# Optimization experiments

Hardware: AMD Instinct MI355X
Metric: run time of the kernel (lower is better)

Reference implementation:

```python
import jax, jax.numpy as jnp
import numpy as np
from jax import lax

# Model hyperparameters (match init_kwargs + Mamba2 defaults: ngroups=1, d_conv=4)
B_, IN_DIM, L_ = 4, 128, 2048
D_MODEL, OUT_DIM, D_STATE, K_SAME = 256, 128, 16, 4
EXPAND, HEADDIM, D_CONV = 3, 3, 4
D_INNER = EXPAND * D_MODEL            # 768
NHEADS = D_INNER // HEADDIM           # 256
CONV_DIM = D_INNER + 2 * D_STATE      # 800 (x, B, C go through depthwise conv)
D_IN_PROJ = 2 * D_INNER + 2 * D_STATE + NHEADS  # 1824 (z, xBC, dt)
EPS = 1e-5
DN = ('NCH', 'OIH', 'NCH')


def setup_inputs() -> dict:
    key = jax.random.key(0)
    ks = jax.random.split(key, 12)
    s = lambda f: 1.0 / np.sqrt(f)
    x = jax.random.normal(ks[0], (B_, IN_DIM, L_), jnp.float32)
    conv_w = jax.random.normal(ks[1], (D_MODEL, IN_DIM, K_SAME), jnp.float32) * s(IN_DIM * K_SAME)
    conv_b = jax.random.normal(ks[2], (D_MODEL,), jnp.float32) * 0.02
    in_proj_w = jax.random.normal(ks[3], (D_MODEL, D_IN_PROJ), jnp.float32) * s(D_MODEL)
    dw_conv_w = jax.random.normal(ks[4], (CONV_DIM, D_CONV), jnp.float32) * s(D_CONV)
    dw_conv_b = jax.random.normal(ks[5], (CONV_DIM,), jnp.float32) * 0.02
    dt_bias = jax.random.normal(ks[6], (NHEADS,), jnp.float32) * 0.5
    A_log = jnp.log(jax.random.uniform(ks[7], (NHEADS,), jnp.float32, 1.0, 16.0))
    D = 1.0 + jax.random.normal(ks[8], (NHEADS,), jnp.float32) * 0.1
    norm_w = jnp.ones((D_INNER,), jnp.float32)
    mamba_out_w = jax.random.normal(ks[9], (D_INNER, D_MODEL), jnp.float32) * s(D_INNER)
    out_conv_w = jax.random.normal(ks[10], (OUT_DIM, D_MODEL, K_SAME), jnp.float32) * s(D_MODEL * K_SAME)
    return dict(x=x, conv_w=conv_w, conv_b=conv_b, in_proj_w=in_proj_w,
                dw_conv_w=dw_conv_w, dw_conv_b=dw_conv_b, dt_bias=dt_bias,
                A_log=A_log, D=D, norm_w=norm_w, mamba_out_w=mamba_out_w,
                out_conv_w=out_conv_w)


def _ssd_scan(dt, A, Bm, Cm, xs):
    """Selective state-space recurrence.
    dt: [B,L,H]  A: [H]  Bm,Cm: [B,L,N]  xs: [B,L,H,P]  ->  y: [B,L,H,P]"""
    dA = jnp.exp(dt * A)  # [B,L,H]

    def step(h, inp):  # h: [B,H,P,N]
        dA_t, dt_t, B_t, C_t, x_t = inp
        dBx = (dt_t[:, :, None] * x_t)[..., None] * B_t[:, None, None, :]  # [B,H,P,N]
        h = h * dA_t[:, :, None, None] + dBx
        y = jnp.einsum('bhpn,bn->bhp', h, C_t)
        return h, y

    inputs = (dA.transpose(1, 0, 2), dt.transpose(1, 0, 2),
              Bm.transpose(1, 0, 2), Cm.transpose(1, 0, 2), xs.transpose(1, 0, 2, 3))
    h0 = jnp.zeros((dt.shape[0], NHEADS, HEADDIM, D_STATE), dt.dtype)
    _, ys = lax.scan(step, h0, inputs)
    return ys.transpose(1, 0, 2, 3)


def reference(x, conv_w, conv_b, in_proj_w, dw_conv_w, dw_conv_b, dt_bias,
              A_log, D, norm_w, mamba_out_w, out_conv_w):
    B, _, L = x.shape
    # Conv1d padding='same' with even kernel k=4: torch pads (left=1, right=2)
    h = lax.conv_general_dilated(x, conv_w, (1,), [(1, 2)], dimension_numbers=DN)
    h = h + conv_b[None, :, None]
    u = h.transpose(0, 2, 1)  # [B,L,d_model]

    zxbcdt = u @ in_proj_w  # [B,L,1824]
    z = zxbcdt[..., :D_INNER]
    xBC = zxbcdt[..., D_INNER:D_INNER + CONV_DIM]
    dt = zxbcdt[..., D_INNER + CONV_DIM:]  # [B,L,H]
    dt = jax.nn.softplus(dt + dt_bias)

    # causal depthwise conv over xBC, then silu
    xBC_c = lax.conv_general_dilated(xBC.transpose(0, 2, 1), dw_conv_w[:, None, :], (1,),
                                     [(D_CONV - 1, 0)], feature_group_count=CONV_DIM,
                                     dimension_numbers=DN)
    xBC = jax.nn.silu((xBC_c + dw_conv_b[None, :, None]).transpose(0, 2, 1))
    xs = xBC[..., :D_INNER].reshape(B, L, NHEADS, HEADDIM)
    Bm = xBC[..., D_INNER:D_INNER + D_STATE]
    Cm = xBC[..., D_INNER + D_STATE:]

    A = -jnp.exp(A_log)
    y = _ssd_scan(dt, A, Bm, Cm, xs) + D[None, None, :, None] * xs  # [B,L,H,P]
    y = y.reshape(B, L, D_INNER)

    # gated RMSNorm (norm_before_gate=False): gate first, then normalize
    y = y * jax.nn.silu(z)
    y = y * lax.rsqrt(jnp.mean(y * y, axis=-1, keepdims=True) + EPS) * norm_w

    out = (y @ mamba_out_w).transpose(0, 2, 1)  # [B,d_model,L]
    out = lax.conv_general_dilated(out, out_conv_w, (1,), [(1, 2)], dimension_numbers=DN)
    return out
```

## Files before the change

### kernel.cpp

```cpp
#include <hip/hip_runtime.h>
#include <math.h>

#define B_      4
#define L_      2048
#define IN_DIM  128
#define D_MODEL 256
#define OUT_DIM 128
#define D_STATE 16
#define D_INNER 768
#define NHEADS  256
#define HEADDIM 3
#define CONV_DIM 800
#define D_IN_PROJ 1824
#define DT_START (D_INNER + CONV_DIM)

#define SCAN_NC 32
#define SCAN_CL 64
#define LPAD    2051

typedef short  short8 __attribute__((ext_vector_type(8)));
typedef float  f32x4  __attribute__((ext_vector_type(4)));

__device__ __forceinline__ unsigned short f2bf(float f) {
    unsigned int u = __float_as_uint(f);
    u = (u + 0x7fffu + ((u >> 16) & 1u)) >> 16;
    return (unsigned short)u;
}
__device__ __forceinline__ float bf2f(unsigned short h) {
    return __uint_as_float(((unsigned int)h) << 16);
}

__global__ __launch_bounds__(256) void prep_all_kernel(
    unsigned short* __restrict__ xh, unsigned short* __restrict__ xl,
    const float* __restrict__ cw, unsigned short* __restrict__ cwh,
    unsigned short* __restrict__ cwl,
    const float* __restrict__ x,
    const float* __restrict__ ipsrc, unsigned short* __restrict__ ipwh,
    unsigned short* __restrict__ ipwl,
    const float* __restrict__ cow, unsigned short* __restrict__ cowh,
    unsigned short* __restrict__ th,
    const float* __restrict__ mosrc, unsigned short* __restrict__ mowh,
    unsigned short* __restrict__ mowl)
{
    __shared__ float tile[32][33];
    int bid = blockIdx.x;
    if (bid < 6) {
        int t = bid * 256 + threadIdx.x;
        int n = B_ * 3 * IN_DIM;
        if (t < n) {
            int ch = t % IN_DIM, rb = t / IN_DIM;
            int b = rb / 3, ri = rb % 3;
            int row = (ri == 0) ? 0 : (ri == 1) ? (L_ + 1) : (L_ + 2);
            size_t off = ((size_t)b * LPAD + row) * IN_DIM + ch;
            xh[off] = 0; xl[off] = 0;
        }
    } else if (bid < 518) {
        int t = (bid - 6) * 256 + threadIdx.x;
        if (t < D_MODEL * 512) {
            int o = t >> 9, kk = t & 511;
            int k = kk >> 7, i = kk & 127;
            float v = cw[((size_t)o * IN_DIM + i) * 4 + k];
            unsigned short h = f2bf(v);
            cwh[t] = h; cwl[t] = f2bf(v - bf2f(h));
        }
    } else if (bid < 1542) {
        int tid = bid - 518;
        int b = tid >> 8;
        int l0 = (tid & 63) * 32, i0 = ((tid >> 6) & 3) * 32;
        int tx = threadIdx.x & 31, ty = threadIdx.x >> 5;
        const float* xb = x + (size_t)b * IN_DIM * L_;
        #pragma unroll
        for (int r = 0; r < 4; ++r)
            tile[ty + r * 8][tx] = xb[(size_t)(i0 + ty + r * 8) * L_ + l0 + tx];
        __syncthreads();
        #pragma unroll
        for (int r = 0; r < 4; ++r) {
            int l = l0 + ty + r * 8;
            float v = tile[tx][ty + r * 8];
            size_t off = ((size_t)b * LPAD + l + 1) * IN_DIM + i0 + tx;
            unsigned short h = f2bf(v);
            xh[off] = h;
            xl[off] = f2bf(v - bf2f(h));
        }
    } else if (bid < 1998) {
        int tid = bid - 1542;
        int n0 = (tid % 57) * 32, k0 = (tid / 57) * 32;
        const int K = D_MODEL, N = D_IN_PROJ;
        int tx = threadIdx.x & 31, ty = threadIdx.x >> 5;
        #pragma unroll
        for (int r = 0; r < 4; ++r)
            tile[ty + r * 8][tx] = ipsrc[(size_t)(k0 + ty + r * 8) * N + n0 + tx];
        __syncthreads();
        #pragma unroll
        for (int r = 0; r < 4; ++r) {
            int n = n0 + ty + r * 8;
            float v = tile[tx][ty + r * 8];
            unsigned short h = f2bf(v);
            ipwh[(size_t)n * K + k0 + tx] = h;
            ipwl[(size_t)n * K + k0 + tx] = f2bf(v - bf2f(h));
        }
    } else if (bid < 2510) {
        int t = (bid - 1998) * 256 + threadIdx.x;
        if (t < OUT_DIM * 1024) {
            int o = t >> 10, kk = t & 1023;
            int k = kk >> 8, c = kk & 255;
            cowh[t] = f2bf(cow[((size_t)o * D_MODEL + c) * 4 + k]);
        }
    } else if (bid < 2522) {
        int t = (bid - 2510) * 256 + threadIdx.x;
        int n = B_ * 3 * D_MODEL;
        if (t < n) {
            int ch = t % D_MODEL, rb = t / D_MODEL;
            int b = rb / 3, ri = rb % 3;
            int row = (ri == 0) ? 0 : (ri == 1) ? (L_ + 1) : (L_ + 2);
            size_t off = ((size_t)b * LPAD + row) * D_MODEL + ch;
            th[off] = 0;
        }
    } else {
        int tid = bid - 2522;
        int n0 = (tid & 7) * 32, k0 = (tid >> 3) * 32;
        const int K = D_INNER, N = D_MODEL;
        int tx = threadIdx.x & 31, ty = threadIdx.x >> 5;
        #pragma unroll
        for (int r = 0; r < 4; ++r)
            tile[ty + r * 8][tx] = mosrc[(size_t)(k0 + ty + r * 8) * N + n0 + tx];
        __syncthreads();
        #pragma unroll
        for (int r = 0; r < 4; ++r) {
            int n = n0 + ty + r * 8;
            float v = tile[tx][ty + r * 8];
            unsigned short h = f2bf(v);
            mowh[(size_t)n * K + k0 + tx] = h;
            mowl[(size_t)n * K + k0 + tx] = f2bf(v - bf2f(h));
        }
    }
}

__global__ __launch_bounds__(256) void gemm_ip2_kernel(
    const unsigned short* __restrict__ Ah, const unsigned short* __restrict__ Al,
    const unsigned short* __restrict__ Bh, const unsigned short* __restrict__ Bl,
    float* __restrict__ C, int M, int N, int K)
{
    __shared__ __align__(16) unsigned short AsH[128][40];
    __shared__ __align__(16) unsigned short AsL[128][40];
    __shared__ __align__(16) unsigned short BsH[128][40];
    __shared__ __align__(16) unsigned short BsL[128][40];

    int m0 = blockIdx.y * 128, n0 = blockIdx.x * 128;
    int t = threadIdx.x;
    int wid = t >> 6, lane = t & 63;
    int wm = (wid >> 1) * 64, wn = (wid & 1) * 64;
    int fr = lane & 15, fq = lane >> 4;
    bool full = (n0 + 127 >= DT_START);

    f32x4 z4 = {0.f, 0.f, 0.f, 0.f};
    f32x4 acc[4][4];
    #pragma unroll
    for (int i = 0; i < 4; ++i)
        #pragma unroll
        for (int j = 0; j < 4; ++j) acc[i][j] = z4;

    if (!full) {
        for (int k0 = 0; k0 < K; k0 += 32) {
            __syncthreads();
            #pragma unroll
            for (int p = 0; p < 2; ++p) {
                int idx = p * 256 + t;
                int row = idx >> 2, q = idx & 3;
                int koff = k0 + q * 8;
                *(float4*)&AsH[row][q * 8] =
                    *(const float4*)(Ah + (size_t)(m0 + row) * K + koff);
                int n = n0 + row;
                *(float4*)&BsH[row][q * 8] =
                    *(const float4*)(Bh + (size_t)n * K + koff);
            }
            __syncthreads();

            short8 ah[4], bh[4];
            #pragma unroll
            for (int i = 0; i < 4; ++i) {
                ah[i] = *(const short8*)&AsH[wm + i * 16 + fr][fq * 8];
                bh[i] = *(const short8*)&BsH[wn + i * 16 + fr][fq * 8];
            }
            #pragma unroll
            for (int i = 0; i < 4; ++i)
                #pragma unroll
                for (int j = 0; j < 4; ++j)
                    acc[i][j] = __builtin_amdgcn_mfma_f32_16x16x32_bf16(
                        ah[i], bh[j], acc[i][j], 0, 0, 0);
        }
    } else {
        for (int k0 = 0; k0 < K; k0 += 32) {
            __syncthreads();
            #pragma unroll
            for (int p = 0; p < 2; ++p) {
                int idx = p * 256 + t;
                int row = idx >> 2, q = idx & 3;
                int koff = k0 + q * 8;
                *(float4*)&AsH[row][q * 8] =
                    *(const float4*)(Ah + (size_t)(m0 + row) * K + koff);
                *(float4*)&AsL[row][q * 8] =
                    *(const float4*)(Al + (size_t)(m0 + row) * K + koff);
                int n = n0 + row;
                float4 vbh = make_float4(0.f, 0.f, 0.f, 0.f), vbl = vbh;
                if (n < N) {
                    vbh = *(const float4*)(Bh + (size_t)n * K + koff);
                    vbl = *(const float4*)(Bl + (size_t)n * K + koff);
                }
                *(float4*)&BsH[row][q * 8] = vbh;
                *(float4*)&BsL[row][q * 8] = vbl;
            }
            __syncthreads();

            short8 ah[4], al[4], bh[4], bl[4];
            #pragma unroll
            for (int i = 0; i < 4; ++i) {
                ah[i] = *(const short8*)&AsH[wm + i * 16 + fr][fq * 8];
                al[i] = *(const short8*)&AsL[wm + i * 16 + fr][fq * 8];
                bh[i] = *(const short8*)&BsH[wn + i * 16 + fr][fq * 8];
                bl[i] = *(const short8*)&BsL[wn + i * 16 + fr][fq * 8];
            }
            #pragma unroll
            for (int i = 0; i < 4; ++i)
                #pragma unroll
                for (int j = 0; j < 4; ++j) {
                    acc[i][j] = __builtin_amdgcn_mfma_f32_16x16x32_bf16(
                        ah[i], bh[j], acc[i][j], 0, 0, 0);
                    acc[i][j] = __builtin_amdgcn_mfma_f32_16x16x32_bf16(
                        ah[i], bl[j], acc[i][j], 0, 0, 0);
                    acc[i][j] = __builtin_amdgcn_mfma_f32_16x16x32_bf16(
                        al[i], bh[j], acc[i][j], 0, 0, 0);
                }
        }
    }

    #pragma unroll
    for (int i = 0; i < 4; ++i) {
        int r0 = m0 + wm + i * 16 + fq * 4;
        #pragma unroll
        for (int j = 0; j < 4; ++j) {
            int cc = n0 + wn + j * 16 + fr;
            if (cc < N) {
                #pragma unroll
                for (int r = 0; r < 4; ++r)
                    C[(size_t)(r0 + r) * N + cc] = acc[i][j][r];
            }
        }
    }
}

__global__ __launch_bounds__(256) void gemm_ci_kernel(
    const unsigned short* __restrict__ Ah, const unsigned short* __restrict__ Al,
    const unsigned short* __restrict__ Bh, const unsigned short* __restrict__ Bl,
    const float* __restrict__ bias,
    unsigned short* __restrict__ Ch, unsigned short* __restrict__ Cl)
{
    const int K = 512;
    __shared__ __align__(16) unsigned short AsH[64][40];
    __shared__ __align__(16) unsigned short AsL[64][40];
    __shared__ __align__(16) unsigned short BsH[128][40];
    __shared__ __align__(16) unsigned short BsL[128][40];

    int m0 = blockIdx.y * 64, n0 = blockIdx.x * 128;
    int b = m0 >> 11;
    size_t abase = ((size_t)b * LPAD + (m0 & 2047)) * IN_DIM;
    int t = threadIdx.x;
    int wid = t >> 6, lane = t & 63;
    int wm = (wid >> 1) * 32, wn = (wid & 1) * 64;
    int fr = lane & 15, fq = lane >> 4;
    int rr = t >> 2, q = t & 3;

    f32x4 z4 = {0.f, 0.f, 0.f, 0.f};
    f32x4 acc[2][4];
    #pragma unroll
    for (int i = 0; i < 2; ++i)
        #pragma unroll
        for (int j = 0; j < 4; ++j) acc[i][j] = z4;

    float4 rAh, rAl, rBh0, rBh1, rBl0, rBl1;
    auto ld = [&](int k0) {
        int koff = k0 + q * 8;
        rAh = *(const float4*)(Ah + abase + (size_t)rr * IN_DIM + koff);
        rAl = *(const float4*)(Al + abase + (size_t)rr * IN_DIM + koff);
        rBh0 = *(const float4*)(Bh + (size_t)(n0 + rr) * K + koff);
        rBh1 = *(const float4*)(Bh + (size_t)(n0 + rr + 64) * K + koff);
        rBl0 = *(const float4*)(Bl + (size_t)(n0 + rr) * K + koff);
        rBl1 = *(const float4*)(Bl + (size_t)(n0 + rr + 64) * K + koff);
    };
    ld(0);

    for (int k0 = 0; k0 < K; k0 += 32) {
        __syncthreads();
        *(float4*)&AsH[rr][q * 8] = rAh;
        *(float4*)&AsL[rr][q * 8] = rAl;
        *(float4*)&BsH[rr][q * 8] = rBh0;
        *(float4*)&BsH[rr + 64][q * 8] = rBh1;
        *(float4*)&BsL[rr][q * 8] = rBl0;
        *(float4*)&BsL[rr + 64][q * 8] = rBl1;
        __syncthreads();
        if (k0 + 32 < K) ld(k0 + 32);

        short8 ah[2], al[2], bh[4], bl[4];
        #pragma unroll
        for (int i = 0; i < 2; ++i) {
            ah[i] = *(const short8*)&AsH[wm + i * 16 + fr][fq * 8];
            al[i] = *(const short8*)&AsL[wm + i * 16 + fr][fq * 8];
        }
        #pragma unroll
        for (int j = 0; j < 4; ++j) {
            bh[j] = *(const short8*)&BsH[wn + j * 16 + fr][fq * 8];
            bl[j] = *(const short8*)&BsL[wn + j * 16 + fr][fq * 8];
        }
        #pragma unroll
        for (int i = 0; i < 2; ++i)
            #pragma unroll
            for (int j = 0; j < 4; ++j) {
                acc[i][j] = __builtin_amdgcn_mfma_f32_16x16x32_bf16(
                    ah[i], bh[j], acc[i][j], 0, 0, 0);
                acc[i][j] = __builtin_amdgcn_mfma_f32_16x16x32_bf16(
                    ah[i], bl[j], acc[i][j], 0, 0, 0);
                acc[i][j] = __builtin_amdgcn_mfma_f32_16x16x32_bf16(
                    al[i], bh[j], acc[i][j], 0, 0, 0);
            }
    }

    #pragma unroll
    for (int i = 0; i < 2; ++i) {
        int r0 = m0 + wm + i * 16 + fq * 4;
        #pragma unroll
        for (int j = 0; j < 4; ++j) {
            int cc = n0 + wn + j * 16 + fr;
            float bc = bias[cc];
            #pragma unroll
            for (int r = 0; r < 4; ++r) {
                float v = acc[i][j][r] + bc;
                unsigned short h = f2bf(v);
                size_t off = (size_t)(r0 + r) * D_MODEL + cc;
                Ch[off] = h;
                Cl[off] = f2bf(v - bf2f(h));
            }
        }
    }
}

__global__ __launch_bounds__(256) void gemm_mo_kernel(
    const unsigned short* __restrict__ Ah, const unsigned short* __restrict__ Bh,
    unsigned short* __restrict__ Ch)
{
    const int K = D_INNER;
    __shared__ __align__(16) unsigned short AsH[64][40];
    __shared__ __align__(16) unsigned short BsH[128][40];

    int m0 = blockIdx.y * 64, n0 = blockIdx.x * 128;
    int t = threadIdx.x;
    int wid = t >> 6, lane = t & 63;
    int wm = (wid >> 1) * 32, wn = (wid & 1) * 64;
    int fr = lane & 15, fq = lane >> 4;
    int rr = t >> 2, q = t & 3;

    f32x4 z4 = {0.f, 0.f, 0.f, 0.f};
    f32x4 acc[2][4];
    #pragma unroll
    for (int i = 0; i < 2; ++i)
        #pragma unroll
        for (int j = 0; j < 4; ++j) acc[i][j] = z4;

    float4 rA, rB0, rB1;
    auto ld = [&](int k0) {
        int koff = k0 + q * 8;
        rA  = *(const float4*)(Ah + (size_t)(m0 + rr) * K + koff);
        rB0 = *(const float4*)(Bh + (size_t)(n0 + rr) * K + koff);
        rB1 = *(const float4*)(Bh + (size_t)(n0 + rr + 64) * K + koff);
    };
    ld(0);

    for (int k0 = 0; k0 < K; k0 += 32) {
        __syncthreads();
        *(float4*)&AsH[rr][q * 8] = rA;
        *(float4*)&BsH[rr][q * 8] = rB0;
        *(float4*)&BsH[rr + 64][q * 8] = rB1;
        __syncthreads();
        if (k0 + 32 < K) ld(k0 + 32);

        short8 ah[2], bh[4];
        #pragma unroll
        for (int i = 0; i < 2; ++i)
            ah[i] = *(const short8*)&AsH[wm + i * 16 + fr][fq * 8];
        #pragma unroll
        for (int j = 0; j < 4; ++j)
            bh[j] = *(const short8*)&BsH[wn + j * 16 + fr][fq * 8];
        #pragma unroll
        for (int i = 0; i < 2; ++i)
            #pragma unroll
            for (int j = 0; j < 4; ++j)
                acc[i][j] = __builtin_amdgcn_mfma_f32_16x16x32_bf16(
                    ah[i], bh[j], acc[i][j], 0, 0, 0);
    }

    int b = m0 >> 11;
    #pragma unroll
    for (int i = 0; i < 2; ++i) {
        int r0 = m0 + wm + i * 16 + fq * 4;
        #pragma unroll
        for (int j = 0; j < 4; ++j) {
            int cc = n0 + wn + j * 16 + fr;
            #pragma unroll
            for (int r = 0; r < 4; ++r) {
                int l = (r0 + r) & 2047;
                size_t off = ((size_t)b * LPAD + l + 1) * D_MODEL + cc;
                Ch[off] = f2bf(acc[i][j][r]);
            }
        }
    }
}

__global__ __launch_bounds__(256) void gemm_co_kernel(
    const unsigned short* __restrict__ Ah, const unsigned short* __restrict__ Bh,
    float* __restrict__ out)
{
    const int K = 1024;
    __shared__ __align__(16) unsigned short AsH[64][40];
    __shared__ __align__(16) unsigned short BsH[64][40];
    __shared__ __align__(16) float outT[64][68];

    int m0 = blockIdx.y * 64, n0 = blockIdx.x * 64;
    int b = m0 >> 11, l0t = m0 & 2047;
    size_t abase = ((size_t)b * LPAD + l0t) * D_MODEL;
    int t = threadIdx.x;
    int wid = t >> 6, lane = t & 63;
    int wm = (wid >> 1) * 32, wn = (wid & 1) * 32;
    int fr = lane & 15, fq = lane >> 4;
    int rr = t >> 2, q = t & 3;

    f32x4 z4 = {0.f, 0.f, 0.f, 0.f};
    f32x4 acc[2][2];
    #pragma unroll
    for (int i = 0; i < 2; ++i)
        #pragma unroll
        for (int j = 0; j < 2; ++j) acc[i][j] = z4;

    float4 rA, rB;
    auto ld = [&](int k0) {
        int koff = k0 + q * 8;
        rA = *(const float4*)(Ah + abase + (size_t)rr * D_MODEL + koff);
        rB = *(const float4*)(Bh + (size_t)(n0 + rr) * K + koff);
    };
    ld(0);

    for (int k0 = 0; k0 < K; k0 += 32) {
        __syncthreads();
        *(float4*)&AsH[rr][q * 8] = rA;
        *(float4*)&BsH[rr][q * 8] = rB;
        __syncthreads();
        if (k0 + 32 < K) ld(k0 + 32);

        short8 ah[2], bh[2];
        #pragma unroll
        for (int i = 0; i < 2; ++i)
            ah[i] = *(const short8*)&AsH[wm + i * 16 + fr][fq * 8];
        #pragma unroll
        for (int j = 0; j < 2; ++j)
            bh[j] = *(const short8*)&BsH[wn + j * 16 + fr][fq * 8];
        #pragma unroll
        for (int i = 0; i < 2; ++i)
            #pragma unroll
            for (int j = 0; j < 2; ++j)
                acc[i][j] = __builtin_amdgcn_mfma_f32_16x16x32_bf16(
                    ah[i], bh[j], acc[i][j], 0, 0, 0);
    }

    #pragma unroll
    for (int i = 0; i < 2; ++i)
        #pragma unroll
        for (int j = 0; j < 2; ++j)
            *(float4*)&outT[wn + j * 16 + fr][wm + i * 16 + fq * 4] =
                make_float4(acc[i][j][0], acc[i][j][1],
                            acc[i][j][2], acc[i][j][3]);
    __syncthreads();
    #pragma unroll
    for (int e = 0; e < 4; ++e) {
        int idx = e * 256 + t;
        int rowl = idx >> 4, colp = (idx & 15) * 4;
        float* dst = out + ((size_t)(b * OUT_DIM + n0 + rowl)) * L_ + l0t + colp;
        *(float4*)dst = *(const float4*)&outT[rowl][colp];
    }
}

__global__ __launch_bounds__(256) void dwconv_kernel(
    const float* __restrict__ zx, const float* __restrict__ w,
    const float* __restrict__ bias, float* __restrict__ xBCs)
{
    int idx = blockIdx.x * 256 + threadIdx.x;
    int c   = idx % CONV_DIM;
    int bl8 = idx / CONV_DIM;
    int b  = bl8 >> 8;
    int l0 = (bl8 & 255) * 8;
    float4 wv = *(const float4*)&w[c * 4];
    float bi = bias[c];
    const float* base = zx + ((size_t)(b * L_ + l0)) * D_IN_PROJ + D_INNER + c;
    float r[11];
    #pragma unroll
    for (int k = 0; k < 11; ++k) {
        int l = l0 - 3 + k;
        r[k] = (l >= 0) ? base[(ptrdiff_t)(k - 3) * D_IN_PROJ] : 0.f;
    }
    #pragma unroll
    for (int i = 0; i < 8; ++i) {
        float acc = bi;
        acc = fmaf(r[i + 0], wv.x, acc);
        acc = fmaf(r[i + 1], wv.y, acc);
        acc = fmaf(r[i + 2], wv.z, acc);
        acc = fmaf(r[i + 3], wv.w, acc);
        float s = acc / (1.f + expf(-acc));
        xBCs[((size_t)(b * L_ + l0 + i)) * CONV_DIM + c] = s;
    }
}

__device__ __forceinline__ void scan_decode(int bid, int& b, int& c, int& hg)
{
    int bcl = bid & 7;
    hg = (bid >> 3) & 31;
    int bc = ((bid >> 8) << 3) | bcl;
    c = bc & 31;
    b = bc >> 5;
}

__global__ __launch_bounds__(512) void scan_local2g(
    const float* __restrict__ xBCs, const float* __restrict__ zx,
    const float* __restrict__ dt_bias, const float* __restrict__ A_log,
    float* __restrict__ Sloc, float* __restrict__ prodA,
    float* __restrict__ dtb, float* __restrict__ G)
{
    int bid = blockIdx.x;
    int t = threadIdx.x;
    if (bid < 128) {
        __shared__ float Bs[64][16];
        __shared__ float Csg[64][16];
        int c = bid & 31, b = bid >> 5;
        int row0 = b * L_ + c * SCAN_CL;
        if (t < 256) {
            int j = t >> 2, q = t & 3;
            const float* r = xBCs + (size_t)(row0 + j) * CONV_DIM + D_INNER;
            *(float4*)&Bs[j][q * 4] = *(const float4*)(r + q * 4);
            *(float4*)&Csg[j][q * 4] = *(const float4*)(r + D_STATE + q * 4);
        }
        __syncthreads();
        if (t < 256) {
            int i = t >> 2, jq = t & 3;
            float4 c0 = *(const float4*)&Csg[i][0];
            float4 c1 = *(const float4*)&Csg[i][4];
            float4 c2 = *(const float4*)&Csg[i][8];
            float4 c3 = *(const float4*)&Csg[i][12];
            float dot[16];
            #pragma unroll
            for (int jj = 0; jj < 16; ++jj) {
                int j = jq * 16 + jj;
                float4 b0 = *(const float4*)&Bs[j][0];
                float4 b1 = *(const float4*)&Bs[j][4];
                float4 b2 = *(const float4*)&Bs[j][8];
                float4 b3 = *(const float4*)&Bs[j][12];
                float d = c0.x * b0.x + c0.y * b0.y + c0.z * b0.z + c0.w * b0.w;
                d = fmaf(c1.x, b1.x, d); d = fmaf(c1.y, b1.y, d);
                d = fmaf(c1.z, b1.z, d); d = fmaf(c1.w, b1.w, d);
                d = fmaf(c2.x, b2.x, d); d = fmaf(c2.y, b2.y, d);
                d = fmaf(c2.z, b2.z, d); d = fmaf(c2.w, b2.w, d);
                d = fmaf(c3.x, b3.x, d); d = fmaf(c3.y, b3.y, d);
                d = fmaf(c3.z, b3.z, d); d = fmaf(c3.w, b3.w, d);
                dot[jj] = d;
            }
            float* gout = G + ((size_t)bid * 64 + i) * 64 + jq * 16;
            #pragma unroll
            for (int q = 0; q < 4; ++q)
                *(float4*)(gout + q * 4) =
                    make_float4(dot[q*4], dot[q*4+1], dot[q*4+2], dot[q*4+3]);
        }
        return;
    }

    __shared__ float  BsT[16][68];
    __shared__ __align__(16) float4 PkC4L[8][66];
    __shared__ float  UT[8][3][64];
    int b, c, hg;
    scan_decode(bid - 128, b, c, hg);
    int h0 = hg * 8;
    int row0 = b * L_ + c * SCAN_CL;

    if (t < 256) {
        int j = t >> 2, q = t & 3;
        const float* r = xBCs + (size_t)(row0 + j) * CONV_DIM;
        float4 bv = *(const float4*)(r + D_INNER + q * 4);
        BsT[q*4+0][j] = bv.x; BsT[q*4+1][j] = bv.y;
        BsT[q*4+2][j] = bv.z; BsT[q*4+3][j] = bv.w;
    }
    {
        int hh = t & 7, j = t >> 3;
        float v = zx[(size_t)(row0 + j) * D_IN_PROJ + DT_START + h0 + hh]
                  + dt_bias[h0 + hh];
        float dtv = (v > 20.f) ? v : log1pf(expf(v));
        dtb[(size_t)(row0 + j) * NHEADS + h0 + hh] = dtv;
        const float* xr = xBCs + (size_t)(row0 + j) * CONV_DIM + (h0 + hh) * 3;
        PkC4L[hh][j] = make_float4(dtv * xr[0], dtv * xr[1], dtv * xr[2], dtv);
    }
    __syncthreads();

    int wv = t >> 6, lane = t & 63;
    int hh = wv;
    int hhu = __builtin_amdgcn_readfirstlane(wv);
    int p = lane >> 4, n = lane & 15;
    int pc = (p < 3) ? p : 2;

    float4 own = PkC4L[hh][lane];
    float pkx = own.x, pky = own.y, pkz = own.z, pkw = own.w;
    float A = -__expf(A_log[h0 + hhu]);
    float cum = pkw * A;
    #pragma unroll
    for (int off = 1; off < 64; off <<= 1) {
        float sv = __shfl_up(cum, off);
        if (lane >= off) cum += sv;
    }
    float cum63 = __shfl(cum, 63);
    float wf = __expf(cum63 - cum);
    UT[hh][0][lane] = wf * pkx;
    UT[hh][1][lane] = wf * pky;
    UT[hh][2][lane] = wf * pkz;
    float state = 0.f;
    #pragma unroll
    for (int q = 0; q < 16; ++q) {
        float4 Bv = *(const float4*)&BsT[n][q * 4];
        float4 Uv = *(const float4*)&UT[hh][pc][q * 4];
        state = fmaf(Uv.x, Bv.x, state);
        state = fmaf(Uv.y, Bv.y, state);
        state = fmaf(Uv.z, Bv.z, state);
        state = fmaf(Uv.w, Bv.w, state);
    }
    size_t bh = (size_t)(b * NHEADS + h0 + hh);
    if (p < 3) Sloc[(bh * SCAN_NC + c) * 48 + p * 16 + n] = state;
    if (lane == 0) prodA[bh * SCAN_NC + c] = __expf(cum63);
}

__global__ __launch_bounds__(256) void scan_prefix_kernel(
    float* __restrict__ Sloc, const float* __restrict__ prodA)
{
    int wv   = blockIdx.x * 4 + (threadIdx.x >> 6);
    int lane = threadIdx.x & 63;
    int p = lane >> 4, n = lane & 15;
    bool act = (p < 3);
    int l48 = ((p < 3) ? p : 2) * 16 + n;
    size_t base = (size_t)wv * SCAN_NC;

    float cur = 0.f;
    for (int c = 0; c < SCAN_NC; ++c) {
        float s  = Sloc[(base + c) * 48 + l48];
        float pa = prodA[base + c];
        if (act) Sloc[(base + c) * 48 + l48] = cur;
        cur = fmaf(pa, cur, s);
    }
}

__global__ __launch_bounds__(512) void scan_final2(
    const float* __restrict__ xBCs, const float* __restrict__ dtb,
    const float* __restrict__ A_log, const float* __restrict__ Dp,
    const float* __restrict__ Sinit, const float* __restrict__ G,
    float* __restrict__ y)
{
    __shared__ __align__(16) float4 PkC4[8][67];
    __shared__ float XWx[8][64];
    __shared__ float XWy[8][64];
    __shared__ float XWz[8][64];
    __shared__ __align__(16) float Cs[64][36];
    union GsYsr {
        float gs[64][64];
        float ysr[64][25];
    };
    __shared__ __align__(16) GsYsr Us;
    int b, c, hg;
    scan_decode(blockIdx.x, b, c, hg);
    int h0 = hg * 8;
    int t = threadIdx.x;
    int row0 = b * L_ + c * SCAN_CL;

    {
        int hh = t & 7, j = t >> 3;
        float dtv = dtb[(size_t)(row0 + j) * NHEADS + h0 + hh];
        const float* xr = xBCs + (size_t)(row0 + j) * CONV_DIM + (h0 + hh) * 3;
        PkC4[hh][j + (j >> 4)] =
            make_float4(dtv * xr[0], dtv * xr[1], dtv * xr[2], dtv);
    }
    if (t < 256) {
        int j = t >> 2, q = t & 3;
        const float* r = xBCs + (size_t)(row0 + j) * CONV_DIM + D_INNER + D_STATE;
        *(float4*)&Cs[j][q * 4] = *(const float4*)(r + q * 4);
    }
    {
        const float* Gsrc = G + (size_t)(b * SCAN_NC + c) * 4096;
        #pragma unroll
        for (int e = 0; e < 2; ++e) {
            int idx = e * 512 + t;
            int row = idx >> 4, cq = (idx & 15) * 4;
            *(float4*)&Us.gs[row][cq ^ ((row & 7) << 2)] =
                *(const float4*)(Gsrc + (size_t)idx * 4);
        }
    }
    __syncthreads();

    int wv = t >> 6, lane = t & 63;
    int hh = wv;
    int hhu = __builtin_amdgcn_readfirstlane(wv);
    int I = lane >> 4;
    int sw = (lane & 7) << 2;

    float4 own = PkC4[hh][lane + (lane >> 4)];
    float pkx = own.x, pky = own.y, pkz = own.z, pkw = own.w;

    const float* sinp = Sinit +
        ((size_t)(b * NHEADS + h0 + hhu) * SCAN_NC + c) * 48;
    float A = -__expf(A_log[h0 + hhu]);
    float Dh = Dp[h0 + hhu];

    float cum = pkw * A;
    #pragma unroll
    for (int off = 1; off < 64; off <<= 1) {
        float sv = __shfl_up(cum, off);
        if (lane >= off) cum += sv;
    }
    float e0 = __shfl(cum, 15);
    float e1 = __shfl(cum, 31);
    float e2 = __shfl(cum, 47);
    float e3 = __shfl(cum, 63);
    int ia = (I << 4) - 1;
    float AIr = __shfl(cum, ia < 0 ? 0 : ia);
    float AI = (I == 0) ? 0.f : AIr;
    float ri = __expf(cum - AI);
    float Eo = (I == 0) ? e0 : (I == 1) ? e1 : (I == 2) ? e2 : e3;
    float wj = __expf(Eo - cum);
    XWx[hh][lane] = wj * pkx;
    XWy[hh][lane] = wj * pky;
    XWz[hh][lane] = wj * pkz;
    PkC4[hh][lane + (lane >> 4)].w = cum;
    float S0 = (I > 0) ? __expf(AI - e0) : 0.f;
    float S1 = (I > 1) ? __expf(AI - e1) : 0.f;
    float S2 = (I > 2) ? __expf(AI - e2) : 0.f;
    float ecum = __expf(cum);

    float4 c0 = *(const float4*)&Cs[lane][0];
    float4 c1 = *(const float4*)&Cs[lane][4];
    float4 c2 = *(const float4*)&Cs[lane][8];
    float4 c3 = *(const float4*)&Cs[lane][12];

    float s0, s1, s2;
    {
        s0 = c0.x*sinp[0];  s0 = fmaf(c0.y,sinp[1],s0);  s0 = fmaf(c0.z,sinp[2],s0);  s0 = fmaf(c0.w,sinp[3],s0);
        s0 = fmaf(c1.x,sinp[4],s0);  s0 = fmaf(c1.y,sinp[5],s0);  s0 = fmaf(c1.z,sinp[6],s0);  s0 = fmaf(c1.w,sinp[7],s0);
        s0 = fmaf(c2.x,sinp[8],s0);  s0 = fmaf(c2.y,sinp[9],s0);  s0 = fmaf(c2.z,sinp[10],s0); s0 = fmaf(c2.w,sinp[11],s0);
        s0 = fmaf(c3.x,sinp[12],s0); s0 = fmaf(c3.y,sinp[13],s0); s0 = fmaf(c3.z,sinp[14],s0); s0 = fmaf(c3.w,sinp[15],s0);
        s1 = c0.x*sinp[16]; s1 = fmaf(c0.y,sinp[17],s1); s1 = fmaf(c0.z,sinp[18],s1); s1 = fmaf(c0.w,sinp[19],s1);
        s1 = fmaf(c1.x,sinp[20],s1); s1 = fmaf(c1.y,sinp[21],s1); s1 = fmaf(c1.z,sinp[22],s1); s1 = fmaf(c1.w,sinp[23],s1);
        s1 = fmaf(c2.x,sinp[24],s1); s1 = fmaf(c2.y,sinp[25],s1); s1 = fmaf(c2.z,sinp[26],s1); s1 = fmaf(c2.w,sinp[27],s1);
        s1 = fmaf(c3.x,sinp[28],s1); s1 = fmaf(c3.y,sinp[29],s1); s1 = fmaf(c3.z,sinp[30],s1); s1 = fmaf(c3.w,sinp[31],s1);
        s2 = c0.x*sinp[32]; s2 = fmaf(c0.y,sinp[33],s2); s2 = fmaf(c0.z,sinp[34],s2); s2 = fmaf(c0.w,sinp[35],s2);
        s2 = fmaf(c1.x,sinp[36],s2); s2 = fmaf(c1.y,sinp[37],s2); s2 = fmaf(c1.z,sinp[38],s2); s2 = fmaf(c1.w,sinp[39],s2);
        s2 = fmaf(c2.x,sinp[40],s2); s2 = fmaf(c2.y,sinp[41],s2); s2 = fmaf(c2.z,sinp[42],s2); s2 = fmaf(c2.w,sinp[43],s2);
        s2 = fmaf(c3.x,sinp[44],s2); s2 = fmaf(c3.y,sinp[45],s2); s2 = fmaf(c3.z,sinp[46],s2); s2 = fmaf(c3.w,sinp[47],s2);
    }

    float acc0 = 0.f, acc1 = 0.f, acc2 = 0.f;
    #pragma unroll
    for (int J = 0; J < 3; ++J) {
        float SJ = (J == 0) ? S0 : (J == 1) ? S1 : S2;
        float t0 = 0.f, t1 = 0.f, t2 = 0.f;
        #pragma unroll
        for (int q = 0; q < 4; ++q) {
            float4 g4 = *(const float4*)&Us.gs[lane][(J * 16 + q * 4) ^ sw];
            float4 ux = *(const float4*)&XWx[hh][J * 16 + q * 4];
            float4 uy = *(const float4*)&XWy[hh][J * 16 + q * 4];
            float4 uz = *(const float4*)&XWz[hh][J * 16 + q * 4];
            t0 = fmaf(g4.x, ux.x, t0); t1 = fmaf(g4.x, uy.x, t1); t2 = fmaf(g4.x, uz.x, t2);
            t0 = fmaf(g4.y, ux.y, t0); t1 = fmaf(g4.y, uy.y, t1); t2 = fmaf(g4.y, uz.y, t2);
            t0 = fmaf(g4.z, ux.z, t0); t1 = fmaf(g4.z, uy.z, t1); t2 = fmaf(g4.z, uz.z, t2);
            t0 = fmaf(g4.w, ux.w, t0); t1 = fmaf(g4.w, uy.w, t1); t2 = fmaf(g4.w, uz.w, t2);
        }
        acc0 = fmaf(SJ, t0, acc0);
        acc1 = fmaf(SJ, t1, acc1);
        acc2 = fmaf(SJ, t2, acc2);
    }

    float d0 = 0.f, d1 = 0.f, d2 = 0.f;
    const float4* pkr = &PkC4[hh][I * 17];
    int lr = lane & 15;
    #pragma unroll
    for (int q = 0; q < 4; ++q) {
        float4 g4 = *(const float4*)&Us.gs[lane][((I << 4) + q * 4) ^ sw];
        #pragma unroll
        for (int k = 0; k < 4; ++k) {
            int kk = q * 4 + k;
            float4 p4 = pkr[kk];
            float gk = (k == 0) ? g4.x : (k == 1) ? g4.y : (k == 2) ? g4.z : g4.w;
            float e = __expf(cum - p4.w);
            float mg = (kk <= lr) ? e * gk : 0.f;
            d0 = fmaf(mg, p4.x, d0);
            d1 = fmaf(mg, p4.y, d1);
            d2 = fmaf(mg, p4.z, d2);
        }
    }

    float rdt = 1.0f / pkw;
    float y0 = fmaf(ri, acc0, d0) + fmaf(ecum, s0, Dh * (pkx * rdt));
    float y1 = fmaf(ri, acc1, d1) + fmaf(ecum, s1, Dh * (pky * rdt));
    float y2 = fmaf(ri, acc2, d2) + fmaf(ecum, s2, Dh * (pkz * rdt));

    __syncthreads();
    {
        float* yr = &Us.ysr[lane][hh * 3];
        yr[0] = y0; yr[1] = y1; yr[2] = y2;
    }
    __syncthreads();

    {
        int i2 = t >> 3, q2 = t & 7;
        float* dst = y + (size_t)(row0 + i2) * D_INNER + hg * 24 + q2 * 3;
        dst[0] = Us.ysr[i2][q2 * 3 + 0];
        dst[1] = Us.ysr[i2][q2 * 3 + 1];
        dst[2] = Us.ysr[i2][q2 * 3 + 2];
    }
}

__global__ __launch_bounds__(256) void gate_norm_kernel(
    const float* __restrict__ zx, const float* __restrict__ norm_w,
    const float* __restrict__ y, unsigned short* __restrict__ yh)
{
    int bl = blockIdx.x;
    int t  = threadIdx.x;
    const float* zrow = zx + (size_t)bl * D_IN_PROJ;
    const float* yrow = y + (size_t)bl * D_INNER;

    float v[3];
    float ss = 0.f;
    #pragma unroll
    for (int j = 0; j < 3; ++j) {
        int i = t + j * 256;
        float z = zrow[i];
        float s = z / (1.f + expf(-z));
        float val = yrow[i] * s;
        v[j] = val;
        ss += val * val;
    }
    ss += __shfl_xor(ss, 32);
    ss += __shfl_xor(ss, 16);
    ss += __shfl_xor(ss, 8);
    ss += __shfl_xor(ss, 4);
    ss += __shfl_xor(ss, 2);
    ss += __shfl_xor(ss, 1);
    __shared__ float red[4];
    int lane = t & 63, wid = t >> 6;
    if (lane == 0) red[wid] = ss;
    __syncthreads();
    float tot = red[0] + red[1] + red[2] + red[3];
    float rs = rsqrtf(tot * (1.f / D_INNER) + 1e-5f);
    #pragma unroll
    for (int j = 0; j < 3; ++j) {
        int i = t + j * 256;
        float o = v[j] * rs * norm_w[i];
        yh[(size_t)bl * D_INNER + i] = f2bf(o);
    }
}

extern "C" void kernel_launch(void* const* d_in, const int* in_sizes, int n_in,
                              void* d_out, int out_size, void* d_ws, size_t ws_size,
                              hipStream_t stream)
{
    const float* x           = (const float*)d_in[0];
    const float* conv_w      = (const float*)d_in[1];
    const float* conv_b      = (const float*)d_in[2];
    const float* in_proj_w   = (const float*)d_in[3];
    const float* dw_conv_w   = (const float*)d_in[4];
    const float* dw_conv_b   = (const float*)d_in[5];
    const float* dt_bias     = (const float*)d_in[6];
    const float* A_log       = (const float*)d_in[7];
    const float* Dp          = (const float*)d_in[8];
    const float* norm_w      = (const float*)d_in[9];
    const float* mamba_out_w = (const float*)d_in[10];
    const float* out_conv_w  = (const float*)d_in[11];
    float* out = (float*)d_out;
    float* ws  = (float*)d_ws;

    float* S0   = ws;
    float* zx   = S0 + 2097152;
    float* xBCs = zx + 14942208;
    float* dtb  = xBCs + 6553600;
    float* ybuf = dtb + 2097152;
    float* tmpPf = ybuf + 6291456;
    float* mowf  = tmpPf + 1050112;
    float* cowf  = mowf + 196608;

    float* Gbuf = S0;
    float* Sloc = S0 + 524288;

    unsigned short* xT_hi = (unsigned short*)zx;
    unsigned short* xT_lo = (unsigned short*)(zx + 525056);
    unsigned short* cw_hi = (unsigned short*)(zx + 1050112);
    unsigned short* cw_lo = (unsigned short*)(zx + 1115648);

    unsigned short* ipw_hi = (unsigned short*)xBCs;
    unsigned short* ipw_lo = (unsigned short*)(xBCs + 233472);
    unsigned short* yb_hi  = (unsigned short*)xBCs;

    float* prodA = ybuf;
    unsigned short* u_hi = (unsigned short*)(ybuf + 32768);
    unsigned short* u_lo = (unsigned short*)(ybuf + 32768 + 1048576);

    unsigned short* tmpP_hi = (unsigned short*)tmpPf;
    unsigned short* mow_hi  = (unsigned short*)mowf;
    unsigned short* mow_lo  = (unsigned short*)(mowf + 98304);
    unsigned short* cow_hi  = (unsigned short*)cowf;

    prep_all_kernel<<<2714, 256, 0, stream>>>(
        xT_hi, xT_lo, conv_w, cw_hi, cw_lo, x, in_proj_w, ipw_hi, ipw_lo,
        out_conv_w, cow_hi, tmpP_hi, mamba_out_w, mow_hi, mow_lo);

    gemm_ci_kernel<<<dim3(2, (B_ * L_) / 64), 256, 0, stream>>>(
        xT_hi, xT_lo, cw_hi, cw_lo, conv_b, u_hi, u_lo);

    gemm_ip2_kernel<<<dim3((D_IN_PROJ + 127) / 128, (B_ * L_) / 128), 256, 0, stream>>>(
        u_hi, u_lo, ipw_hi, ipw_lo, zx, B_ * L_, D_IN_PROJ, D_MODEL);

    dwconv_kernel<<<(B_ * (L_ / 8) * CONV_DIM) / 256, 256, 0, stream>>>(
        zx, dw_conv_w, dw_conv_b, xBCs);
    scan_local2g<<<128 + B_ * SCAN_NC * (NHEADS / 8), 512, 0, stream>>>(
        xBCs, zx, dt_bias, A_log, Sloc, prodA, dtb, Gbuf);
    scan_prefix_kernel<<<(B_ * NHEADS) / 4, 256, 0, stream>>>(Sloc, prodA);
    scan_final2<<<B_ * SCAN_NC * (NHEADS / 8), 512, 0, stream>>>(
        xBCs, dtb, A_log, Dp, Sloc, Gbuf, ybuf);

    gate_norm_kernel<<<B_ * L_, 256, 0, stream>>>(zx, norm_w, ybuf, yb_hi);

    gemm_mo_kernel<<<dim3(2, (B_ * L_) / 64), 256, 0, stream>>>(
        yb_hi, mow_hi, tmpP_hi);

    gemm_co_kernel<<<dim3(OUT_DIM / 64, (B_ * L_) / 64), 256, 0, stream>>>(
        tmpP_hi, cow_hi, out);
}
```

Before: 238.0 us.

## Fuse gated RMSNorm into mamba out-projection GEMM prologue

Removes the separate gate_norm kernel and computes silu gating, norm_w scaling and the per-row RMS inside the out-projection GEMM, staging the whole 16x768 bf16 A tile in LDS. The per-row rsqrt is applied to the accumulator in the epilogue instead of before bf16 rounding. This drops one launch and the bf16 intermediate round trip through global memory. In exchange, tiles shrink to 16 rows by 256 columns, so each block rereads the whole weight matrix and the grid has far more blocks.

```diff
diff --git a/kernel.cpp b/kernel.cpp
--- a/kernel.cpp
+++ b/kernel.cpp
@@ -343,73 +343,109 @@
     }
 }
 
-__global__ __launch_bounds__(256) void gemm_mo_kernel(
-    const unsigned short* __restrict__ Ah, const unsigned short* __restrict__ Bh,
+__global__ __launch_bounds__(256) void gemm_mog_kernel(
+    const float* __restrict__ ybuf, const float* __restrict__ zx,
+    const float* __restrict__ norm_w,
+    const unsigned short* __restrict__ Bh,
     unsigned short* __restrict__ Ch)
 {
     const int K = D_INNER;
-    __shared__ __align__(16) unsigned short AsH[64][40];
-    __shared__ __align__(16) unsigned short BsH[128][40];
-
-    int m0 = blockIdx.y * 64, n0 = blockIdx.x * 128;
+    __shared__ __align__(16) unsigned short Alds[16][776];
+    __shared__ __align__(16) unsigned short Bs[256][40];
+    __shared__ float rs_l[16];
+
+    int m0 = blockIdx.x * 16;
     int t = threadIdx.x;
     int wid = t >> 6, lane = t & 63;
-    int wm = (wid >> 1) * 32, wn = (wid & 1) * 64;
+
+    {
+        float nw0[6], nw1[6];
+        #pragma unroll
+        for (int s = 0; s < 6; ++s) {
+            float2 nw = *(const float2*)&norm_w[2 * lane + 128 * s];
+            nw0[s] = nw.x; nw1[s] = nw.y;
+        }
+        #pragma unroll
+        for (int rr = 0; rr < 4; ++rr) {
+            int r = wid * 4 + rr;
+            const float* yr = ybuf + (size_t)(m0 + r) * D_INNER;
+            const float* zr = zx + (size_t)(m0 + r) * D_IN_PROJ;
+            float ss = 0.f;
+            unsigned int pk[6];
+            #pragma unroll
+            for (int s = 0; s < 6; ++s) {
+                int c0 = 2 * lane + 128 * s;
+                float2 yv = *(const float2*)&yr[c0];
+                float2 zv = *(const float2*)&zr[c0];
+                float v0 = yv.x * (zv.x / (1.f + expf(-zv.x)));
+                float v1 = yv.y * (zv.y / (1.f + expf(-zv.y)));
+                ss += v0 * v0 + v1 * v1;
+                pk[s] = (unsigned int)f2bf(v0 * nw0[s])
+                      | ((unsigned int)f2bf(v1 * nw1[s]) << 16);
+            }
+            #pragma unroll
+            for (int s = 0; s < 6; ++s)
+                *(unsigned int*)&Alds[r][2 * lane + 128 * s] = pk[s];
+            ss += __shfl_xor(ss, 32);
+            ss += __shfl_xor(ss, 16);
+            ss += __shfl_xor(ss, 8);
+            ss += __shfl_xor(ss, 4);
+            ss += __shfl_xor(ss, 2);
+            ss += __shfl_xor(ss, 1);
+            if (lane == 0)
+                rs_l[r] = rsqrtf(ss * (1.f / D_INNER) + 1e-5f);
+        }
+    }
+
     int fr = lane & 15, fq = lane >> 4;
-    int rr = t >> 2, q = t & 3;
+    int wn = wid * 64;
 
     f32x4 z4 = {0.f, 0.f, 0.f, 0.f};
-    f32x4 acc[2][4];
-    #pragma unroll
-    for (int i = 0; i < 2; ++i)
-        #pragma unroll
-        for (int j = 0; j < 4; ++j) acc[i][j] = z4;
-
-    float4 rA, rB0, rB1;
-    auto ld = [&](int k0) {
-        int koff = k0 + q * 8;
-        rA  = *(const float4*)(Ah + (size_t)(m0 + rr) * K + koff);
-        rB0 = *(const float4*)(Bh + (size_t)(n0 + rr) * K + koff);
-        rB1 = *(const float4*)(Bh + (size_t)(n0 + rr + 64) * K + koff);
+    f32x4 acc[4] = {z4, z4, z4, z4};
+
+    float4 rB[4];
+    auto ldB = [&](int k0) {
+        #pragma unroll
+        for (int p = 0; p < 4; ++p) {
+            int idx = p * 256 + t;
+            int row = idx >> 2, q = idx & 3;
+            rB[p] = *(const float4*)(Bh + (size_t)row * K + k0 + q * 8);
+        }
     };
-    ld(0);
+    ldB(0);
 
     for (int k0 = 0; k0 < K; k0 += 32) {
         __syncthreads();
-        *(float4*)&AsH[rr][q * 8] = rA;
-        *(float4*)&BsH[rr][q * 8] = rB0;
-        *(float4*)&BsH[rr + 64][q * 8] = rB1;
+        #pragma unroll
+        for (int p = 0; p < 4; ++p) {
+            int idx = p * 256 + t;
+            int row = idx >> 2, q = idx & 3;
+            *(float4*)&Bs[row][q * 8] = rB[p];
+        }
         __syncthreads();
-        if (k0 + 32 < K) ld(k0 + 32);
-
-        short8 ah[2], bh[4];
-        #pragma unroll
-        for (int i = 0; i < 2; ++i)
-            ah[i] = *(const short8*)&AsH[wm + i * 16 + fr][fq * 8];
+        if (k0 + 32 < K) ldB(k0 + 32);
+
+        short8 a = *(const short8*)&Alds[fr][k0 + fq * 8];
+        short8 bh[4];
         #pragma unroll
         for (int j = 0; j < 4; ++j)
-            bh[j] = *(const short8*)&BsH[wn + j * 16 + fr][fq * 8];
-        #pragma unroll
-        for (int i = 0; i < 2; ++i)
-            #pragma unroll
-            for (int j = 0; j < 4; ++j)
-                acc[i][j] = __builtin_amdgcn_mfma_f32_16x16x32_bf16(
-                    ah[i], bh[j], acc[i][j], 0, 0, 0);
-    }
-
-    int b = m0 >> 11;
-    #pragma unroll
-    for (int i = 0; i < 2; ++i) {
-        int r0 = m0 + wm + i * 16 + fq * 4;
-        #pragma unroll
-        for (int j = 0; j < 4; ++j) {
-            int cc = n0 + wn + j * 16 + fr;
-            #pragma unroll
-            for (int r = 0; r < 4; ++r) {
-                int l = (r0 + r) & 2047;
-                size_t off = ((size_t)b * LPAD + l + 1) * D_MODEL + cc;
-                Ch[off] = f2bf(acc[i][j][r]);
-            }
+            bh[j] = *(const short8*)&Bs[wn + j * 16 + fr][fq * 8];
+        #pragma unroll
+        for (int j = 0; j < 4; ++j)
+            acc[j] = __builtin_amdgcn_mfma_f32_16x16x32_bf16(
+                a, bh[j], acc[j], 0, 0, 0);
+    }
+
+    int b = m0 >> 11, l0t = m0 & 2047;
+    #pragma unroll
+    for (int j = 0; j < 4; ++j) {
+        int cc = wn + j * 16 + fr;
+        #pragma unroll
+        for (int r = 0; r < 4; ++r) {
+            int row = fq * 4 + r;
+            float v = acc[j][r] * rs_l[row];
+            size_t off = ((size_t)b * LPAD + (l0t + row) + 1) * D_MODEL + cc;
+            Ch[off] = f2bf(v);
         }
     }
 }
@@ -824,46 +860,6 @@
     }
 }
 
-__global__ __launch_bounds__(256) void gate_norm_kernel(
-    const float* __restrict__ zx, const float* __restrict__ norm_w,
-    const float* __restrict__ y, unsigned short* __restrict__ yh)
-{
-    int bl = blockIdx.x;
-    int t  = threadIdx.x;
-    const float* zrow = zx + (size_t)bl * D_IN_PROJ;
-    const float* yrow = y + (size_t)bl * D_INNER;
-
-    float v[3];
-    float ss = 0.f;
-    #pragma unroll
-    for (int j = 0; j < 3; ++j) {
-        int i = t + j * 256;
-        float z = zrow[i];
-        float s = z / (1.f + expf(-z));
-        float val = yrow[i] * s;
-        v[j] = val;
-        ss += val * val;
-    }
-    ss += __shfl_xor(ss, 32);
-    ss += __shfl_xor(ss, 16);
-    ss += __shfl_xor(ss, 8);
-    ss += __shfl_xor(ss, 4);
-    ss += __shfl_xor(ss, 2);
-    ss += __shfl_xor(ss, 1);
-    __shared__ float red[4];
-    int lane = t & 63, wid = t >> 6;
-    if (lane == 0) red[wid] = ss;
-    __syncthreads();
-    float tot = red[0] + red[1] + red[2] + red[3];
-    float rs = rsqrtf(tot * (1.f / D_INNER) + 1e-5f);
-    #pragma unroll
-    for (int j = 0; j < 3; ++j) {
-        int i = t + j * 256;
-        float o = v[j] * rs * norm_w[i];
-        yh[(size_t)bl * D_INNER + i] = f2bf(o);
-    }
-}
-
 extern "C" void kernel_launch(void* const* d_in, const int* in_sizes, int n_in,
                               void* d_out, int out_size, void* d_ws, size_t ws_size,
                               hipStream_t stream)
@@ -902,7 +898,6 @@
 
     unsigned short* ipw_hi = (unsigned short*)xBCs;
     unsigned short* ipw_lo = (unsigned short*)(xBCs + 233472);
-    unsigned short* yb_hi  = (unsigned short*)xBCs;
 
     float* prodA = ybuf;
     unsigned short* u_hi = (unsigned short*)(ybuf + 32768);
@@ -931,10 +926,8 @@
     scan_final2<<<B_ * SCAN_NC * (NHEADS / 8), 512, 0, stream>>>(
         xBCs, dtb, A_log, Dp, Sloc, Gbuf, ybuf);
 
-    gate_norm_kernel<<<B_ * L_, 256, 0, stream>>>(zx, norm_w, ybuf, yb_hi);
-
-    gemm_mo_kernel<<<dim3(2, (B_ * L_) / 64), 256, 0, stream>>>(
-        yb_hi, mow_hi, tmpP_hi);
+    gemm_mog_kernel<<<(B_ * L_) / 16, 256, 0, stream>>>(
+        ybuf, zx, norm_w, mow_hi, tmpP_hi);
 
     gemm_co_kernel<<<dim3(OUT_DIM / 64, (B_ * L_) / 64), 256, 0, stream>>>(
         tmpP_hi, cow_hi, out);
```

Measured after the change: 280.0 us. 1.18x slower.

## Fuse gated RMSNorm into the mamba out-projection GEMM prologue

Applied to the files above, without the earlier changes.

Drops the separate gate_norm kernel. The out-projection GEMM now loads fp32 y and z directly, applies the SiLU gate and norm weight while staging A tiles, and accumulates the per-row sum of squares. Because the RMS scale is constant per row, it is applied to the accumulator in the epilogue. This removes one launch and the bf16 round-trip of the normalized activations. In exchange, each of the two N-blocks recomputes the gate (expf) and rereads y/z, and the loop does more work per K step.

```diff
diff --git a/kernel.cpp b/kernel.cpp
--- a/kernel.cpp
+++ b/kernel.cpp
@@ -343,13 +343,17 @@
     }
 }
 
-__global__ __launch_bounds__(256) void gemm_mo_kernel(
-    const unsigned short* __restrict__ Ah, const unsigned short* __restrict__ Bh,
+__global__ __launch_bounds__(256) void gemm_mog2_kernel(
+    const float* __restrict__ ybuf, const float* __restrict__ zx,
+    const float* __restrict__ norm_w,
+    const unsigned short* __restrict__ Bh,
     unsigned short* __restrict__ Ch)
 {
     const int K = D_INNER;
-    __shared__ __align__(16) unsigned short AsH[64][40];
-    __shared__ __align__(16) unsigned short BsH[128][40];
+    __shared__ __align__(16) unsigned short As[64][40];
+    __shared__ __align__(16) unsigned short Bs[128][40];
+    __shared__ __align__(16) float nws[768];
+    __shared__ float rs_l[64];
 
     int m0 = blockIdx.y * 64, n0 = blockIdx.x * 128;
     int t = threadIdx.x;
@@ -358,6 +362,8 @@
     int fr = lane & 15, fq = lane >> 4;
     int rr = t >> 2, q = t & 3;
 
+    if (t < 192) *(float4*)&nws[t * 4] = *(const float4*)&norm_w[t * 4];
+
     f32x4 z4 = {0.f, 0.f, 0.f, 0.f};
     f32x4 acc[2][4];
     #pragma unroll
@@ -365,30 +371,57 @@
         #pragma unroll
         for (int j = 0; j < 4; ++j) acc[i][j] = z4;
 
-    float4 rA, rB0, rB1;
-    auto ld = [&](int k0) {
+    const float* yrow = ybuf + (size_t)(m0 + rr) * D_INNER;
+    const float* zrow = zx + (size_t)(m0 + rr) * D_IN_PROJ;
+
+    float ss = 0.f;
+    unsigned int pk0, pk1, pk2, pk3;
+    float4 rB0, rB1;
+    auto ldg = [&](int k0) {
         int koff = k0 + q * 8;
-        rA  = *(const float4*)(Ah + (size_t)(m0 + rr) * K + koff);
+        float4 y0 = *(const float4*)(yrow + koff);
+        float4 y1 = *(const float4*)(yrow + koff + 4);
+        float4 zv0 = *(const float4*)(zrow + koff);
+        float4 zv1 = *(const float4*)(zrow + koff + 4);
         rB0 = *(const float4*)(Bh + (size_t)(n0 + rr) * K + koff);
         rB1 = *(const float4*)(Bh + (size_t)(n0 + rr + 64) * K + koff);
+        float4 nw0 = *(const float4*)&nws[koff];
+        float4 nw1 = *(const float4*)&nws[koff + 4];
+        float v0 = y0.x * (zv0.x / (1.f + expf(-zv0.x)));
+        float v1 = y0.y * (zv0.y / (1.f + expf(-zv0.y)));
+        float v2 = y0.z * (zv0.z / (1.f + expf(-zv0.z)));
+        float v3 = y0.w * (zv0.w / (1.f + expf(-zv0.w)));
+        float v4 = y1.x * (zv1.x / (1.f + expf(-zv1.x)));
+        float v5 = y1.y * (zv1.y / (1.f + expf(-zv1.y)));
+        float v6 = y1.z * (zv1.z / (1.f + expf(-zv1.z)));
+        float v7 = y1.w * (zv1.w / (1.f + expf(-zv1.w)));
+        ss += v0*v0 + v1*v1 + v2*v2 + v3*v3 + v4*v4 + v5*v5 + v6*v6 + v7*v7;
+        pk0 = (unsigned int)f2bf(v0 * nw0.x) | ((unsigned int)f2bf(v1 * nw0.y) << 16);
+        pk1 = (unsigned int)f2bf(v2 * nw0.z) | ((unsigned int)f2bf(v3 * nw0.w) << 16);
+        pk2 = (unsigned int)f2bf(v4 * nw1.x) | ((unsigned int)f2bf(v5 * nw1.y) << 16);
+        pk3 = (unsigned int)f2bf(v6 * nw1.z) | ((unsigned int)f2bf(v7 * nw1.w) << 16);
     };
-    ld(0);
+    __syncthreads();
+    ldg(0);
 
     for (int k0 = 0; k0 < K; k0 += 32) {
         __syncthreads();
-        *(float4*)&AsH[rr][q * 8] = rA;
-        *(float4*)&BsH[rr][q * 8] = rB0;
-        *(float4*)&BsH[rr + 64][q * 8] = rB1;
+        {
+            unsigned int* ap = (unsigned int*)&As[rr][q * 8];
+            ap[0] = pk0; ap[1] = pk1; ap[2] = pk2; ap[3] = pk3;
+        }
+        *(float4*)&Bs[rr][q * 8] = rB0;
+        *(float4*)&Bs[rr + 64][q * 8] = rB1;
         __syncthreads();
-        if (k0 + 32 < K) ld(k0 + 32);
+        if (k0 + 32 < K) ldg(k0 + 32);
 
         short8 ah[2], bh[4];
         #pragma unroll
         for (int i = 0; i < 2; ++i)
-            ah[i] = *(const short8*)&AsH[wm + i * 16 + fr][fq * 8];
+            ah[i] = *(const short8*)&As[wm + i * 16 + fr][fq * 8];
         #pragma unroll
         for (int j = 0; j < 4; ++j)
-            bh[j] = *(const short8*)&BsH[wn + j * 16 + fr][fq * 8];
+            bh[j] = *(const short8*)&Bs[wn + j * 16 + fr][fq * 8];
         #pragma unroll
         for (int i = 0; i < 2; ++i)
             #pragma unroll
@@ -397,18 +430,26 @@
                     ah[i], bh[j], acc[i][j], 0, 0, 0);
     }
 
+    ss += __shfl_xor(ss, 1);
+    ss += __shfl_xor(ss, 2);
+    if ((lane & 3) == 0)
+        rs_l[rr] = rsqrtf(ss * (1.f / D_INNER) + 1e-5f);
+    __syncthreads();
+
     int b = m0 >> 11;
     #pragma unroll
     for (int i = 0; i < 2; ++i) {
-        int r0 = m0 + wm + i * 16 + fq * 4;
+        int rl0 = wm + i * 16 + fq * 4;
         #pragma unroll
         for (int j = 0; j < 4; ++j) {
             int cc = n0 + wn + j * 16 + fr;
             #pragma unroll
             for (int r = 0; r < 4; ++r) {
-                int l = (r0 + r) & 2047;
+                int rl = rl0 + r;
+                float v = acc[i][j][r] * rs_l[rl];
+                int l = (m0 + rl) & 2047;
                 size_t off = ((size_t)b * LPAD + l + 1) * D_MODEL + cc;
-                Ch[off] = f2bf(acc[i][j][r]);
+                Ch[off] = f2bf(v);
             }
         }
     }
@@ -824,46 +865,6 @@
     }
 }
 
-__global__ __launch_bounds__(256) void gate_norm_kernel(
-    const float* __restrict__ zx, const float* __restrict__ norm_w,
-    const float* __restrict__ y, unsigned short* __restrict__ yh)
-{
-    int bl = blockIdx.x;
-    int t  = threadIdx.x;
-    const float* zrow = zx + (size_t)bl * D_IN_PROJ;
-    const float* yrow = y + (size_t)bl * D_INNER;
-
-    float v[3];
-    float ss = 0.f;
-    #pragma unroll
-    for (int j = 0; j < 3; ++j) {
-        int i = t + j * 256;
-        float z = zrow[i];
-        float s = z / (1.f + expf(-z));
-        float val = yrow[i] * s;
-        v[j] = val;
-        ss += val * val;
-    }
-    ss += __shfl_xor(ss, 32);
-    ss += __shfl_xor(ss, 16);
-    ss += __shfl_xor(ss, 8);
-    ss += __shfl_xor(ss, 4);
-    ss += __shfl_xor(ss, 2);
-    ss += __shfl_xor(ss, 1);
-    __shared__ float red[4];
-    int lane = t & 63, wid = t >> 6;
-    if (lane == 0) red[wid] = ss;
-    __syncthreads();
-    float tot = red[0] + red[1] + red[2] + red[3];
-    float rs = rsqrtf(tot * (1.f / D_INNER) + 1e-5f);
-    #pragma unroll
-    for (int j = 0; j < 3; ++j) {
-        int i = t + j * 256;
-        float o = v[j] * rs * norm_w[i];
-        yh[(size_t)bl * D_INNER + i] = f2bf(o);
-    }
-}
-
 extern "C" void kernel_launch(void* const* d_in, const int* in_sizes, int n_in,
                               void* d_out, int out_size, void* d_ws, size_t ws_size,
                               hipStream_t stream)
@@ -902,7 +903,6 @@
 
     unsigned short* ipw_hi = (unsigned short*)xBCs;
     unsigned short* ipw_lo = (unsigned short*)(xBCs + 233472);
-    unsigned short* yb_hi  = (unsigned short*)xBCs;
 
     float* prodA = ybuf;
     unsigned short* u_hi = (unsigned short*)(ybuf + 32768);
@@ -931,10 +931,8 @@
     scan_final2<<<B_ * SCAN_NC * (NHEADS / 8), 512, 0, stream>>>(
         xBCs, dtb, A_log, Dp, Sloc, Gbuf, ybuf);
 
-    gate_norm_kernel<<<B_ * L_, 256, 0, stream>>>(zx, norm_w, ybuf, yb_hi);
-
-    gemm_mo_kernel<<<dim3(2, (B_ * L_) / 64), 256, 0, stream>>>(
-        yb_hi, mow_hi, tmpP_hi);
+    gemm_mog2_kernel<<<dim3(2, (B_ * L_) / 64), 256, 0, stream>>>(
+        ybuf, zx, norm_w, mow_hi, tmpP_hi);
 
     gemm_co_kernel<<<dim3(OUT_DIM / 64, (B_ * L_) / 64), 256, 0, stream>>>(
         tmpP_hi, cow_hi, out);
```

Result: slower. 252.1 us (+5.9%).
